# Kernel tuning notes

Hardware: AMD Instinct MI355X
Metric: run time of the kernel (lower is better)

## Reference

```python
import jax, jax.numpy as jnp
import numpy as np

B, D_ENC, T = 4, 512, 200
D_DEC, U = 640, 100
H, V = 640, 1025


def setup_inputs() -> dict:
    key = jax.random.key(0)
    ks = jax.random.split(key, 8)
    s = lambda k, shape, fan: jax.random.normal(k, shape, dtype=jnp.float32) / np.sqrt(fan)
    return {
        "encoder_outputs": jax.random.normal(ks[0], (B, D_ENC, T), dtype=jnp.float32),
        "decoder_outputs": jax.random.normal(ks[1], (B, D_DEC, U), dtype=jnp.float32),
        "W_enc": s(ks[2], (D_ENC, H), D_ENC),
        "b_enc": jnp.zeros((H,), dtype=jnp.float32),
        "W_pred": s(ks[3], (D_DEC, H), D_DEC),
        "b_pred": jnp.zeros((H,), dtype=jnp.float32),
        "W_out": s(ks[4], (H, V), H),
        "b_out": jnp.zeros((V,), dtype=jnp.float32),
    }


def reference(encoder_outputs, decoder_outputs, W_enc, b_enc, W_pred, b_pred, W_out, b_out):
    # transpose(1,2): [B, D, T] -> [B, T, D], then linear projections to H
    enc_proj = jnp.einsum("bdt,dh->bth", encoder_outputs, W_enc) + b_enc   # [B, T, H]
    dec_proj = jnp.einsum("bdu,dh->buh", decoder_outputs, W_pred) + b_pred  # [B, U, H]
    # broadcast-sum: [B, T, 1, H] + [B, 1, U, H] -> [B, T, U, H]
    x = enc_proj[:, :, None, :] + dec_proj[:, None, :, :]
    x = jax.nn.relu(x)           # joint_net[0] activation; joint_net[1] dropout = identity (eval)
    out = jnp.einsum("btuh,hv->btuv", x, W_out) + b_out  # [B, T, U, V]
    return out
```

## Files before the change

### kernel.cpp

```cpp
#include <hip/hip_runtime.h>
#include <hip/hip_bf16.h>

#define B_   4
#define DENC 512
#define T_   200
#define DDEC 640
#define U_   100
#define H_   640
#define V_   1025
#define VPAD 1152

typedef float f32x4 __attribute__((ext_vector_type(4)));
typedef _Float16 f16x8 __attribute__((ext_vector_type(8)));

__device__ __forceinline__ uint4 addrelu16(uint4 e, uint4 d) {
    f16x8 ev = __builtin_bit_cast(f16x8, e);
    f16x8 dv = __builtin_bit_cast(f16x8, d);
    f16x8 s = ev + dv;
    f16x8 z = {(_Float16)0.f, (_Float16)0.f, (_Float16)0.f, (_Float16)0.f,
               (_Float16)0.f, (_Float16)0.f, (_Float16)0.f, (_Float16)0.f};
    s = __builtin_elementwise_max(s, z);
    return __builtin_bit_cast(uint4, s);
}

__device__ __forceinline__ void gload_lds16(const void* g, void* l) {
    __builtin_amdgcn_global_load_lds(
        (const __attribute__((address_space(1))) unsigned int*)g,
        (__attribute__((address_space(3))) unsigned int*)l, 16, 0, 0);
}

__global__ __launch_bounds__(512) void prep_fused_kernel(
    const float* __restrict__ enc, const float* __restrict__ W_enc,
    const float* __restrict__ b_enc,
    const float* __restrict__ dec, const float* __restrict__ W_pred,
    const float* __restrict__ b_pred,
    const float* __restrict__ W_out,
    _Float16* __restrict__ encP, _Float16* __restrict__ decP,
    _Float16* __restrict__ Wt)
{
    __shared__ float sbuf[8448];
    int bx = blockIdx.x;
    int tid = threadIdx.x;
    int lane = tid & 63, w = tid >> 6;

    if (bx < 520) {
        int b = bx / 130, r5 = bx % 130, hc = r5 / 13, tg = r5 % 13;
        int h  = hc * 64 + lane;
        int t0 = tg * 16;
        const float* Wc = W_enc + h;
        const float* ec = enc + (size_t)b * DENC * T_ + t0;
        int d0 = w * 64;
        float acc[16];
        #pragma unroll
        for (int i = 0; i < 16; ++i) acc[i] = 0.f;
        if (t0 + 16 <= T_) {
            #pragma unroll 8
            for (int i = 0; i < 64; ++i) {
                int d = d0 + i;
                float wv = Wc[(size_t)d * H_];
                const float* p = ec + (size_t)d * T_;
                float4 a0 = *(const float4*)(p);
                float4 a1 = *(const float4*)(p + 4);
                float4 a2 = *(const float4*)(p + 8);
                float4 a3 = *(const float4*)(p + 12);
                acc[0]+=wv*a0.x; acc[1]+=wv*a0.y; acc[2]+=wv*a0.z; acc[3]+=wv*a0.w;
                acc[4]+=wv*a1.x; acc[5]+=wv*a1.y; acc[6]+=wv*a1.z; acc[7]+=wv*a1.w;
                acc[8]+=wv*a2.x; acc[9]+=wv*a2.y; acc[10]+=wv*a2.z; acc[11]+=wv*a2.w;
                acc[12]+=wv*a3.x; acc[13]+=wv*a3.y; acc[14]+=wv*a3.z; acc[15]+=wv*a3.w;
            }
        } else {
            #pragma unroll 8
            for (int i = 0; i < 64; ++i) {
                int d = d0 + i;
                float wv = Wc[(size_t)d * H_];
                const float* p = ec + (size_t)d * T_;
                float4 a0 = *(const float4*)(p);
                float4 a1 = *(const float4*)(p + 4);
                acc[0]+=wv*a0.x; acc[1]+=wv*a0.y; acc[2]+=wv*a0.z; acc[3]+=wv*a0.w;
                acc[4]+=wv*a1.x; acc[5]+=wv*a1.y; acc[6]+=wv*a1.z; acc[7]+=wv*a1.w;
            }
        }
        #pragma unroll
        for (int t = 0; t < 16; ++t)
            sbuf[(w * 16 + t) * 66 + lane] = acc[t];
        __syncthreads();
        #pragma unroll
        for (int k = 0; k < 2; ++k) {
            int oi = tid + k * 512;
            int t = oi >> 6, hl = oi & 63;
            if (t0 + t < T_) {
                float s = 0.f;
                #pragma unroll
                for (int ww = 0; ww < 8; ++ww)
                    s += sbuf[(ww * 16 + t) * 66 + hl];
                s += b_enc[hc * 64 + hl];
                encP[((size_t)b * T_ + t0 + t) * H_ + hc * 64 + hl] = (_Float16)s;
            }
        }
    } else if (bx < 1040) {
        int i5 = bx - 520;
        int b = i5 / 130, r5 = i5 % 130, hc = r5 / 13, ug = r5 % 13;
        int h  = hc * 64 + lane;
        int u0 = ug * 8;
        const float* Wc = W_pred + h;
        const float* dc = dec + (size_t)b * DDEC * U_ + u0;
        int d0 = w * 80;
        float acc[8];
        #pragma unroll
        for (int i = 0; i < 8; ++i) acc[i] = 0.f;
        if (u0 + 8 <= U_) {
            #pragma unroll 8
            for (int i = 0; i < 80; ++i) {
                int d = d0 + i;
                float wv = Wc[(size_t)d * H_];
                const float* p = dc + (size_t)d * U_;
                float4 a0 = *(const float4*)(p);
                float4 a1 = *(const float4*)(p + 4);
                acc[0]+=wv*a0.x; acc[1]+=wv*a0.y; acc[2]+=wv*a0.z; acc[3]+=wv*a0.w;
                acc[4]+=wv*a1.x; acc[5]+=wv*a1.y; acc[6]+=wv*a1.z; acc[7]+=wv*a1.w;
            }
        } else {
            #pragma unroll 8
            for (int i = 0; i < 80; ++i) {
                int d = d0 + i;
                float wv = Wc[(size_t)d * H_];
                const float* p = dc + (size_t)d * U_;
                float4 a0 = *(const float4*)(p);
                acc[0]+=wv*a0.x; acc[1]+=wv*a0.y; acc[2]+=wv*a0.z; acc[3]+=wv*a0.w;
            }
        }
        #pragma unroll
        for (int u = 0; u < 8; ++u)
            sbuf[(w * 8 + u) * 66 + lane] = acc[u];
        __syncthreads();
        {
            int u = tid >> 6, hl = tid & 63;
            if (u0 + u < U_) {
                float s = 0.f;
                #pragma unroll
                for (int ww = 0; ww < 8; ++ww)
                    s += sbuf[(ww * 8 + u) * 66 + hl];
                s += b_pred[hc * 64 + hl];
                decP[((size_t)b * U_ + u0 + u) * H_ + hc * 64 + hl] = (_Float16)s;
            }
        }
    } else {
        int j = bx - 1040;
        int hc = j / 18, vc = j % 18;
        int h0 = hc * 64, v0 = vc * 64;
        float (*tile)[65] = (float(*)[65])sbuf;
        #pragma unroll
        for (int it = 0; it < 8; ++it) {
            int hl = it * 8 + (tid >> 6);
            int vl = tid & 63;
            int v = v0 + vl;
            tile[hl][vl] = (v < V_) ? W_out[(size_t)(h0 + hl) * V_ + v] : 0.f;
        }
        __syncthreads();
        #pragma unroll
        for (int it = 0; it < 8; ++it) {
            int vl = it * 8 + (tid >> 6);
            int hl = tid & 63;
            Wt[(size_t)(v0 + vl) * H_ + h0 + hl] = (_Float16)tile[hl][vl];
        }
    }
}

#define ESTR 260
__global__ __launch_bounds__(256, 4) void joint_kernel(
    const unsigned short* __restrict__ encP,
    const unsigned short* __restrict__ decP,
    const unsigned short* __restrict__ Wt,
    const float* __restrict__ b_out,
    float* __restrict__ out)
{
    __shared__ uint4 LA[2][64][4];
    __shared__ uint4 LB[2][256][4];
    int tid = threadIdx.x;

    if (blockIdx.x >= 5200) {
        int idx = (blockIdx.x - 5200) * 256 + tid;
        if (idx >= B_ * T_ * U_) return;
        int u = idx % U_;
        int t = (idx / U_) % T_;
        int b = idx / (U_ * T_);
        const uint4* e = (const uint4*)(encP + ((size_t)b * T_ + t) * H_);
        const uint4* d = (const uint4*)(decP + ((size_t)b * U_ + u) * H_);
        const uint4* wv = (const uint4*)(Wt + (size_t)1024 * H_);
        float acc1 = 0.f;
        for (int c = 0; c < H_ / 8; ++c) {
            f16x8 x = __builtin_bit_cast(f16x8, addrelu16(e[c], d[c]));
            f16x8 wq = __builtin_bit_cast(f16x8, wv[c]);
            #pragma unroll
            for (int m = 0; m < 8; ++m)
                acc1 += (float)x[m] * (float)wq[m];
        }
        out[((size_t)(b * T_ + t) * U_ + u) * V_ + 1024] = acc1 + b_out[1024];
        return;
    }

    int f   = blockIdx.x;
    int n   = (f & 7) * 650 + (f >> 3);
    int vi  = n / 1300;
    int rem = n - vi * 1300;
    int b   = rem / 325;
    int tu  = rem - b * 325;

    int tt = tu / 13, ut = tu % 13;
    int t0 = tt * 8, u0 = ut * 8, vb = vi * 256;
    int lane = tid & 63, w = tid >> 6;
    int lrow = lane & 15, kg = lane >> 4;

    int r  = tid >> 2, kc = tid & 3;
    int ta = t0 + (r >> 3);
    int ua = u0 + (r & 7); if (ua > U_ - 1) ua = U_ - 1;
    const unsigned short* eR = encP + ((size_t)b * T_ + ta) * H_ + kc * 8;
    const unsigned short* dR = decP + ((size_t)b * U_ + ua) * H_ + kc * 8;
    int fA = (r >> 1) & 3;

    int pcB = lane & 3;
    const unsigned short* gB[4];
    #pragma unroll
    for (int m = 0; m < 4; ++m) {
        int cl = w * 64 + m * 16 + (lane >> 2);
        gB[m] = Wt + (size_t)(vb + cl) * H_ + (pcB ^ ((cl >> 1) & 3)) * 8;
    }

    f32x4 acc[4][4];
    #pragma unroll
    for (int i = 0; i < 4; ++i)
        #pragma unroll
        for (int j = 0; j < 4; ++j)
            acc[i][j] = (f32x4){0.f, 0.f, 0.f, 0.f};

    {
        uint4 E = *(const uint4*)(eR);
        uint4 D = *(const uint4*)(dR);
        LA[0][r][kc ^ fA] = addrelu16(E, D);
        #pragma unroll
        for (int m = 0; m < 4; ++m)
            gload_lds16(gB[m], &LB[0][w * 64 + m * 16][0]);
    }
    __syncthreads();

    #pragma unroll 2
    for (int kt = 0; kt < 20; ++kt) {
        int cur = kt & 1;
        uint4 En, Dn;
        if (kt < 19) {
            En = *(const uint4*)(eR + (kt + 1) * 32);
            Dn = *(const uint4*)(dR + (kt + 1) * 32);
            #pragma unroll
            for (int m = 0; m < 4; ++m)
                gload_lds16(gB[m] + (kt + 1) * 32, &LB[cur ^ 1][w * 64 + m * 16][0]);
        }
        f16x8 a[4], bq[4];
        #pragma unroll
        for (int i = 0; i < 4; ++i) {
            int row = i * 16 + lrow;
            a[i] = __builtin_bit_cast(f16x8, LA[cur][row][kg ^ ((row >> 1) & 3)]);
        }
        #pragma unroll
        for (int j = 0; j < 4; ++j) {
            int col = w * 64 + j * 16 + lrow;
            bq[j] = __builtin_bit_cast(f16x8, LB[cur][col][kg ^ ((col >> 1) & 3)]);
        }
        #pragma unroll
        for (int i = 0; i < 4; ++i)
            #pragma unroll
            for (int j = 0; j < 4; ++j)
                acc[i][j] = __builtin_amdgcn_mfma_f32_16x16x32_f16(a[i], bq[j], acc[i][j], 0, 0, 0);
        if (kt < 19)
            LA[cur ^ 1][r][kc ^ fA] = addrelu16(En, Dn);
        __syncthreads();
    }

    float* etile = (float*)LB;
    #pragma unroll
    for (int i = 0; i < 4; ++i) {
        __syncthreads();
        #pragma unroll
        for (int j = 0; j < 4; ++j) {
            int col = w * 64 + j * 16 + lrow;
            float bo = b_out[vb + col];
            #pragma unroll
            for (int q = 0; q < 4; ++q)
                etile[(kg * 4 + q) * ESTR + col] = acc[i][j][q] + bo;
        }
        __syncthreads();
        #pragma unroll
        for (int rr = 0; rr < 4; ++rr) {
            int row16 = w * 4 + rr;
            int row = i * 16 + row16;
            int t = t0 + (row >> 3);
            int u = u0 + (row & 7);
            if (u < U_) {
                float* ob = &out[(((size_t)b * T_ + t) * U_ + u) * V_ + vb];
                const float* lb = &etile[row16 * ESTR];
                #pragma unroll
                for (int it = 0; it < 4; ++it)
                    ob[it * 64 + lane] = lb[it * 64 + lane];
            }
        }
    }
}

extern "C" void kernel_launch(void* const* d_in, const int* in_sizes, int n_in,
                              void* d_out, int out_size, void* d_ws, size_t ws_size,
                              hipStream_t stream) {
    const float* enc    = (const float*)d_in[0];
    const float* dec    = (const float*)d_in[1];
    const float* W_enc  = (const float*)d_in[2];
    const float* b_enc  = (const float*)d_in[3];
    const float* W_pred = (const float*)d_in[4];
    const float* b_pred = (const float*)d_in[5];
    const float* W_out  = (const float*)d_in[6];
    const float* b_out  = (const float*)d_in[7];
    float* out = (float*)d_out;

    char* ws = (char*)d_ws;
    _Float16* encP = (_Float16*)ws;
    _Float16* decP = (_Float16*)(ws + 1024000);
    _Float16* Wt   = (_Float16*)(ws + 1024000 + 512000);

    prep_fused_kernel<<<dim3(1220), 512, 0, stream>>>(
        enc, W_enc, b_enc, dec, W_pred, b_pred, W_out, encP, decP, Wt);
    joint_kernel<<<dim3(5200 + (B_ * T_ * U_ + 255) / 256), 256, 0, stream>>>(
        (const unsigned short*)encP, (const unsigned short*)decP,
        (const unsigned short*)Wt, b_out, out);
}
```

Baseline: 235.8 us.

## Enlarge joint GEMM block tile to 128 rows with 512-thread, 2x4 wave grid

Each joint-kernel block now computes 128 (t,u) rows × 256 vocab columns with 8 waves laid out 2×4, instead of 64 rows with 4 waves. Shared memory is flattened into one buffer holding double-buffered A and B tiles, and the epilogue staging tile is reused across both wave rows. Each W_out tile loaded into LDS now serves twice as many rows, cutting global and L2 traffic for W and halving the block count. In exchange, the 16-row t tiles overrun T=200, so some compute is wasted and bounds checks are needed. The larger block also raises register and LDS pressure per CU.

Measured after the change: 238.3 us. About the same (+1.1%).

```diff
diff --git a/kernel.cpp b/kernel.cpp
--- a/kernel.cpp
+++ b/kernel.cpp
@@ -166,20 +166,20 @@
     }
 }
 
-#define ESTR 260
-__global__ __launch_bounds__(256, 4) void joint_kernel(
+__global__ __launch_bounds__(512, 4) void joint_kernel(
     const unsigned short* __restrict__ encP,
     const unsigned short* __restrict__ decP,
     const unsigned short* __restrict__ Wt,
     const float* __restrict__ b_out,
     float* __restrict__ out)
 {
-    __shared__ uint4 LA[2][64][4];
-    __shared__ uint4 LB[2][256][4];
+    __shared__ uint4 LDSu[3072];
+    uint4* LA = LDSu;
+    uint4* LB = LDSu + 1024;
     int tid = threadIdx.x;
 
-    if (blockIdx.x >= 5200) {
-        int idx = (blockIdx.x - 5200) * 256 + tid;
+    if (blockIdx.x >= 2704) {
+        int idx = (blockIdx.x - 2704) * 512 + tid;
         if (idx >= B_ * T_ * U_) return;
         int u = idx % U_;
         int t = (idx / U_) % T_;
@@ -200,29 +200,29 @@
     }
 
     int f   = blockIdx.x;
-    int n   = (f & 7) * 650 + (f >> 3);
-    int vi  = n / 1300;
-    int rem = n - vi * 1300;
-    int b   = rem / 325;
-    int tu  = rem - b * 325;
-
+    int n   = (f & 7) * 338 + (f >> 3);
+    int vi  = n / 676;
+    int rem = n - vi * 676;
+    int b   = rem / 169;
+    int tu  = rem - b * 169;
     int tt = tu / 13, ut = tu % 13;
-    int t0 = tt * 8, u0 = ut * 8, vb = vi * 256;
+    int t0 = tt * 16, u0 = ut * 8, vb = vi * 256;
     int lane = tid & 63, w = tid >> 6;
+    int wr = w >> 2, wc = w & 3;
     int lrow = lane & 15, kg = lane >> 4;
 
     int r  = tid >> 2, kc = tid & 3;
-    int ta = t0 + (r >> 3);
-    int ua = u0 + (r & 7); if (ua > U_ - 1) ua = U_ - 1;
+    int ta = t0 + (r >> 3); if (ta > T_ - 1) ta = T_ - 1;
+    int ua = u0 + (r & 7);  if (ua > U_ - 1) ua = U_ - 1;
     const unsigned short* eR = encP + ((size_t)b * T_ + ta) * H_ + kc * 8;
     const unsigned short* dR = decP + ((size_t)b * U_ + ua) * H_ + kc * 8;
     int fA = (r >> 1) & 3;
 
     int pcB = lane & 3;
-    const unsigned short* gB[4];
+    const unsigned short* gB[2];
     #pragma unroll
-    for (int m = 0; m < 4; ++m) {
-        int cl = w * 64 + m * 16 + (lane >> 2);
+    for (int m = 0; m < 2; ++m) {
+        int cl = w * 32 + m * 16 + (lane >> 2);
         gB[m] = Wt + (size_t)(vb + cl) * H_ + (pcB ^ ((cl >> 1) & 3)) * 8;
     }
 
@@ -236,10 +236,10 @@
     {
         uint4 E = *(const uint4*)(eR);
         uint4 D = *(const uint4*)(dR);
-        LA[0][r][kc ^ fA] = addrelu16(E, D);
-        #pragma unroll
-        for (int m = 0; m < 4; ++m)
-            gload_lds16(gB[m], &LB[0][w * 64 + m * 16][0]);
+        LA[(0 * 128 + r) * 4 + (kc ^ fA)] = addrelu16(E, D);
+        #pragma unroll
+        for (int m = 0; m < 2; ++m)
+            gload_lds16(gB[m], &LB[(size_t)(0 * 256 + w * 32 + m * 16) * 4]);
     }
     __syncthreads();
 
@@ -251,19 +251,20 @@
             En = *(const uint4*)(eR + (kt + 1) * 32);
             Dn = *(const uint4*)(dR + (kt + 1) * 32);
             #pragma unroll
-            for (int m = 0; m < 4; ++m)
-                gload_lds16(gB[m] + (kt + 1) * 32, &LB[cur ^ 1][w * 64 + m * 16][0]);
+            for (int m = 0; m < 2; ++m)
+                gload_lds16(gB[m] + (kt + 1) * 32,
+                            &LB[(size_t)((cur ^ 1) * 256 + w * 32 + m * 16) * 4]);
         }
         f16x8 a[4], bq[4];
         #pragma unroll
         for (int i = 0; i < 4; ++i) {
-            int row = i * 16 + lrow;
-            a[i] = __builtin_bit_cast(f16x8, LA[cur][row][kg ^ ((row >> 1) & 3)]);
+            int row = wr * 64 + i * 16 + lrow;
+            a[i] = __builtin_bit_cast(f16x8, LA[(cur * 128 + row) * 4 + (kg ^ ((row >> 1) & 3))]);
         }
         #pragma unroll
         for (int j = 0; j < 4; ++j) {
-            int col = w * 64 + j * 16 + lrow;
-            bq[j] = __builtin_bit_cast(f16x8, LB[cur][col][kg ^ ((col >> 1) & 3)]);
+            int col = wc * 64 + j * 16 + lrow;
+            bq[j] = __builtin_bit_cast(f16x8, LB[(cur * 256 + col) * 4 + (kg ^ ((col >> 1) & 3))]);
         }
         #pragma unroll
         for (int i = 0; i < 4; ++i)
@@ -271,32 +272,33 @@
             for (int j = 0; j < 4; ++j)
                 acc[i][j] = __builtin_amdgcn_mfma_f32_16x16x32_f16(a[i], bq[j], acc[i][j], 0, 0, 0);
         if (kt < 19)
-            LA[cur ^ 1][r][kc ^ fA] = addrelu16(En, Dn);
-        __syncthreads();
-    }
-
-    float* etile = (float*)LB;
+            LA[((cur ^ 1) * 128 + r) * 4 + (kc ^ fA)] = addrelu16(En, Dn);
+        __syncthreads();
+    }
+
+    float* etile = (float*)LDSu;
     #pragma unroll
     for (int i = 0; i < 4; ++i) {
         __syncthreads();
         #pragma unroll
         for (int j = 0; j < 4; ++j) {
-            int col = w * 64 + j * 16 + lrow;
+            int col = wc * 64 + j * 16 + lrow;
             float bo = b_out[vb + col];
             #pragma unroll
             for (int q = 0; q < 4; ++q)
-                etile[(kg * 4 + q) * ESTR + col] = acc[i][j][q] + bo;
+                etile[(wr * 16 + kg * 4 + q) * 260 + col] = acc[i][j][q] + bo;
         }
         __syncthreads();
         #pragma unroll
         for (int rr = 0; rr < 4; ++rr) {
-            int row16 = w * 4 + rr;
-            int row = i * 16 + row16;
+            int wrs = w >> 2;
+            int r16 = (w & 3) * 4 + rr;
+            int row = wrs * 64 + i * 16 + r16;
             int t = t0 + (row >> 3);
             int u = u0 + (row & 7);
-            if (u < U_) {
+            if (t < T_ && u < U_) {
                 float* ob = &out[(((size_t)b * T_ + t) * U_ + u) * V_ + vb];
-                const float* lb = &etile[row16 * ESTR];
+                const float* lb = &etile[(wrs * 16 + r16) * 260];
                 #pragma unroll
                 for (int it = 0; it < 4; ++it)
                     ob[it * 64 + lane] = lb[it * 64 + lane];
@@ -325,7 +327,7 @@
 
     prep_fused_kernel<<<dim3(1220), 512, 0, stream>>>(
         enc, W_enc, b_enc, dec, W_pred, b_pred, W_out, encP, decP, Wt);
-    joint_kernel<<<dim3(5200 + (B_ * T_ * U_ + 255) / 256), 256, 0, stream>>>(
+    joint_kernel<<<dim3(2704 + 157), 512, 0, stream>>>(
         (const unsigned short*)encP, (const unsigned short*)decP,
         (const unsigned short*)Wt, b_out, out);
 }
```
